# Kernel tuning notes

Measured on AMD Instinct MI355X. Metric: run time of the kernel, lower is better.

The kernel has to match this reference:

```python
import jax, jax.numpy as jnp
import numpy as np

TOTAL_NUM_PROP = 2000   # opt['total_num_prop_gp']
THR_START_END = 0.5     # opt['thr_start_end_gp']
NEG = -1e30             # score for invalid anchors


def setup_inputs() -> dict:
    key = jax.random.key(0)
    k1, k2, k3 = jax.random.split(key, 3)
    B, T = 16, 2048
    return {
        "start": jax.random.uniform(k1, (B, T), jnp.float32),
        "end": jax.random.uniform(k2, (B, T), jnp.float32),
        "actionness": jax.random.uniform(k3, (B, T), jnp.float32),
    }


def _select_anchors(p):
    # local-peak test (rise on left AND fall on right, boundaries count as true)
    # OR above-threshold test; matches uint8 sel1*sel2 + sel3 > 0 in torch code.
    B = p.shape[0]
    pad = jnp.ones((B, 1), bool)
    rise = jnp.concatenate([pad, p[:, 1:] > p[:, :-1]], axis=1)
    fall = jnp.concatenate([p[:, :-1] > p[:, 1:], pad], axis=1)
    high = p > THR_START_END * jnp.max(p, axis=1, keepdims=True)
    return (rise & fall) | high


def reference(start, end, actionness):
    # gen_prop == 'start_end' branch with tscale == T (step == 1)
    B, T = start.shape
    ss = _select_anchors(start)          # [B, T] selected start anchors
    es = _select_anchors(end)            # [B, T] selected end anchors
    s_ax = jnp.arange(T)
    # valid anchor pairs: both selected and end index >= start index
    valid = ss[:, :, None] & es[:, None, :] & (s_ax[None, :, None] <= s_ax[None, None, :])
    scores = jnp.where(valid, start[:, :, None] * end[:, None, :], NEG)  # [B, T, T]
    # per-batch top-K proposals by score (replaces argsort(descending)[:K])
    vals, idx = jax.lax.top_k(scores.reshape(B, T * T), TOTAL_NUM_PROP)
    s_idx = idx // T                      # start position
    e_idx = idx % T                       # end position
    keep = (vals > NEG).astype(jnp.float32)  # guards the (rare) <K-valid case
    dur = e_idx - s_idx                   # duration-minus-1 row index
    b_idx = jnp.broadcast_to(jnp.arange(B)[:, None], s_idx.shape)
    # scatter ones into dense [B, tscale(dur), tscale(start)] indicator map
    out = jnp.zeros((B, T, T), jnp.float32).at[b_idx, dur, s_idx].max(keep)
    return out
```

## Files before the change

### kernel.cpp

```cpp
#include <hip/hip_runtime.h>

constexpr int NB = 16;
constexpr int NT = 2048;
constexpr int KPROP = 2000;
constexpr int CAP = 8192;
constexpr int TIE_CAP = 2048;


__device__ void dscan(const unsigned* __restrict__ h, int nbuck, int nd, int tid,
                      int* cs, int* oB, int* oNd) {
    int chunk = nbuck >> 8;
    if (tid < 256) {
        int base = tid * chunk, s2 = 0;
        for (int c = 0; c < chunk; c++) s2 += (int)h[base + c];
        cs[tid] = s2;
    }
    __syncthreads();
    if (tid == 0) {
        int acc = 0, tc = -1;
        for (int t2 = 255; t2 >= 0; t2--) {
            if (acc + cs[t2] >= nd) { tc = t2; break; }
            acc += cs[t2];
        }
        int found = -1;
        if (tc >= 0) {
            for (int c = tc * chunk + chunk - 1; c >= tc * chunk; c--) {
                int cnt = (int)h[c];
                if (acc + cnt >= nd) { found = c; break; }
                acc += cnt;
            }
        }
        *oB = found;
        *oNd = nd - acc;
    }
    __syncthreads();
}

__device__ int scan512_excl(int x, int tid, volatile int* wsum, int* totOut) {
    int lane = tid & 63, wv = tid >> 6;
    int inc = x;
    #pragma unroll
    for (int d = 1; d < 64; d <<= 1) {
        int y = __shfl_up(inc, d);
        if (lane >= d) inc += y;
    }
    if (lane == 63) wsum[wv] = inc;
    __syncthreads();
    int base = 0, tot = 0;
    for (int w2 = 0; w2 < 8; w2++) {
        int v2 = wsum[w2];
        if (w2 < wv) base += v2;
        tot += v2;
    }
    __syncthreads();
    *totOut = tot;
    return base + (inc - x);
}

__device__ int reduce512(int x, int tid, volatile int* wsum) {
    int lane = tid & 63, wv = tid >> 6;
    #pragma unroll
    for (int d = 32; d > 0; d >>= 1) x += __shfl_down(x, d);
    if (lane == 0) wsum[wv] = x;
    __syncthreads();
    int tot = 0;
    for (int w2 = 0; w2 < 8; w2++) tot += wsum[w2];
    __syncthreads();
    return tot;
}

__global__ __launch_bounds__(512) void k_main(
        const float* __restrict__ start, const float* __restrict__ end,
        float4* __restrict__ out4,
        int* __restrict__ gMode, unsigned* __restrict__ gV32,
        int* __restrict__ gNd2, int* __restrict__ gCnt,
        unsigned* __restrict__ candFlat, unsigned* __restrict__ candBits) {
    int blk = blockIdx.x, tid = threadIdx.x;
    if (blk >= NB) {
        float4 z = make_float4(0.f, 0.f, 0.f, 0.f);
        size_t base = (size_t)(blk - NB) * 8192 + tid;
        #pragma unroll
        for (int it = 0; it < 16; it++) out4[base + (size_t)it * 512] = z;
        return;
    }
    int b = blk;
    size_t bc = (size_t)b * CAP;

    __shared__ short lsI[NT];  __shared__ float lsV[NT];
    __shared__ short leI[NT];  __shared__ float evV[NT];
    __shared__ float evVs[NT]; __shared__ short evIs[NT];
    __shared__ short actI[NT]; __shared__ short actC[NT];
    __shared__ unsigned Pmut[2048];
    __shared__ short PE[2051];
    __shared__ float redS[8];
    __shared__ int   red8[8];
    __shared__ int   cs[256];
    __shared__ float sMaxA[2];
    __shared__ int   sN[2];
    __shared__ int   scnt, sB, sNd;

    int lane = tid & 63, wv = tid >> 6;

    int w = tid >> 8, t = tid & 255;
    const float* p = (w ? end : start) + (size_t)b * NT;

    int t0 = t * 8;
    float v[8];
    *(float4*)&v[0] = *(const float4*)&p[t0];
    *(float4*)&v[4] = *(const float4*)&p[t0 + 4];

    float m = v[0];
    #pragma unroll
    for (int k = 1; k < 8; k++) m = fmaxf(m, v[k]);
    #pragma unroll
    for (int d = 32; d > 0; d >>= 1) m = fmaxf(m, (float)__shfl_down(m, d));
    if (lane == 0) redS[wv] = m;
    __syncthreads();
    float rowMax = fmaxf(fmaxf(redS[w * 4 + 0], redS[w * 4 + 1]),
                         fmaxf(redS[w * 4 + 2], redS[w * 4 + 3]));
    float thr = 0.5f * rowMax;
    if (t == 0) sMaxA[w] = rowMax;

    float prev = (t == 0)   ? -1.0f : p[t0 - 1];
    float next = (t == 255) ? -1.0f : p[t0 + 8];

    bool flag[8];
    int c = 0;
    #pragma unroll
    for (int k = 0; k < 8; k++) {
        float pv = (k == 0) ? prev : v[k - 1];
        float nv = (k == 7) ? next : v[k + 1];
        bool f = ((v[k] > pv) && (v[k] > nv)) || (v[k] > thr);
        flag[k] = f;
        c += f;
    }
    int inc = c;
    #pragma unroll
    for (int d = 1; d < 64; d <<= 1) {
        int y = __shfl_up(inc, d);
        if (lane >= d) inc += y;
    }
    if (lane == 63) red8[wv] = inc;
    __syncthreads();
    int base0 = 0;
    #pragma unroll
    for (int q = 0; q < 4; q++) {
        int vq = red8[w * 4 + q];
        if (q < (t >> 6)) base0 += vq;
    }
    int halfTot = red8[w * 4] + red8[w * 4 + 1] + red8[w * 4 + 2] + red8[w * 4 + 3];
    int pos = base0 + (inc - c);
    #pragma unroll
    for (int k = 0; k < 8; k++) {
        if (flag[k]) {
            if (w == 0) { lsI[pos] = (short)(t0 + k); lsV[pos] = v[k]; }
            else        { leI[pos] = (short)(t0 + k); evV[pos] = v[k]; }
            pos++;
        }
    }
    if (t == 0) sN[w] = halfTot;
    __syncthreads();

    int mS = sN[0], mE = sN[1];
    float maxE = sMaxA[1];
    float maxP = sMaxA[0] * maxE;

    int myTot = 0;
    for (int i = tid; i < mS; i += 512) {
        int sPos = lsI[i];
        int lo2 = 0, hi2 = mE;
        while (lo2 < hi2) { int mid = (lo2 + hi2) >> 1; if (leI[mid] < sPos) lo2 = mid + 1; else hi2 = mid; }
        myTot += mE - lo2;
    }
    int totalValid = reduce512(myTot, tid, red8);

    if (totalValid < KPROP) {
        if (tid == 0) scnt = 0;
        __syncthreads();
        for (int i = wv; i < mS; i += 8) {
            int sPos = lsI[i];
            for (int jb = 0; jb < mE; jb += 64) {
                int j = jb + lane;
                bool tk = (j < mE) && ((int)leI[j] >= sPos);
                unsigned long long vm = __ballot(tk);
                int cntv = __popcll(vm);
                if (cntv) {
                    int bw = 0;
                    if (lane == 0) bw = atomicAdd(&scnt, cntv);
                    bw = __shfl(bw, 0);
                    if (tk) {
                        int p2 = bw + __popcll(vm & ((1ull << lane) - 1ull));
                        if (p2 < CAP) candFlat[bc + p2] = (unsigned)((sPos << 11) | (int)leI[j]);
                    }
                }
            }
        }
        __syncthreads();
        if (tid == 0) { gMode[b] = 2; gCnt[b] = min(scnt, CAP); }
        return;
    }

    float mn = 3.4e38f;
    for (int k = tid; k < mE; k += 512) mn = fminf(mn, evV[k]);
    #pragma unroll
    for (int d = 32; d > 0; d >>= 1) mn = fminf(mn, (float)__shfl_down(mn, d));
    if (lane == 0) redS[wv] = mn;
    __syncthreads();
    float minV = redS[0];
    for (int w2 = 1; w2 < 8; w2++) minV = fminf(minV, redS[w2]);
    __syncthreads();
    float invW = 2047.0f / fmaxf(maxE - minV, 1e-30f);

    for (int k = tid; k < 2048; k += 512) Pmut[k] = 0u;
    __syncthreads();
    for (int k = tid; k < mE; k += 512) {
        float kf = fminf((evV[k] - minV) * invW, 2047.0f);
        int key = (int)kf; if (key < 0) key = 0;
        atomicAdd(&Pmut[2047 - key], 1u);
    }
    __syncthreads();
    {
        int c4[4], sum4 = 0;
        #pragma unroll
        for (int q = 0; q < 4; q++) { c4[q] = (int)Pmut[tid * 4 + q]; sum4 += c4[q]; }
        int tot;
        int base = scan512_excl(sum4, tid, red8, &tot);
        int run = base;
        #pragma unroll
        for (int q = 0; q < 4; q++) { PE[tid * 4 + q] = (short)run; run += c4[q]; }
        if (tid == 0) { PE[2048] = (short)tot; PE[2049] = (short)mE; PE[2050] = (short)mE; }
    }
    __syncthreads();
    for (int k = tid; k < 2048; k += 512) Pmut[k] = (unsigned)(short)PE[k];
    __syncthreads();
    for (int k = tid; k < mE; k += 512) {
        float vE = evV[k];
        float kf = fminf((vE - minV) * invW, 2047.0f);
        int key = (int)kf; if (key < 0) key = 0;
        int p2 = (int)atomicAdd(&Pmut[2047 - key], 1u);
        evVs[p2] = vE; evIs[p2] = leI[k];
    }
    __syncthreads();

    auto rowCount = [&](float tau, float sv) -> int {
        float x = tau / sv;
        float kf = fminf((x - minV) * invW, 2050.0f);
        int kk = (int)kf - 2;
        if (kk < -2) kk = -2;
        if (kk > 2048) kk = 2048;
        return (int)PE[2048 - kk];
    };
    auto incOracle = [&](float tau) -> int {
        int my = 0;
        for (int i = tid; i < mS; i += 512) my += rowCount(tau, lsV[i]);
        return reduce512(my, tid, red8);
    };

    float aT = 0.0f, bT = maxP;
    float Fa = (float)mS * (float)mE;
    float Fb = 0.0f;
    float t40 = -1.0f;
    for (int it = 0; it < 12; it++) {
        float mid;
        float denom = Fa - Fb;
        if (denom > 1.0f) {
            mid = aT + (bT - aT) * ((Fa - 9000.0f) / denom);
            if (!(mid > aT && mid < bT)) mid = 0.5f * (aT + bT);
        } else mid = 0.5f * (aT + bT);
        int incC = incOracle(mid);
        if (incC > 13000) { aT = mid; Fa = (float)incC; }
        else if (incC < 5000) { bT = mid; Fb = (float)incC; }
        else { t40 = mid; break; }
    }
    if (t40 < 0.0f && Fa <= 24576.0f) t40 = aT;

    bool ok = false;
    int n = 0;

    if (t40 >= 0.0f) {
        __shared__ int sActN;
        {
            int a4[4], na = 0;
            #pragma unroll
            for (int q = 0; q < 4; q++) {
                int i = tid * 4 + q;
                int C = (i < mS) ? rowCount(t40, lsV[i]) : 0;
                a4[q] = C; na += (C > 0);
            }
            int tot;
            int base = scan512_excl(na, tid, red8, &tot);
            int run = base;
            #pragma unroll
            for (int q = 0; q < 4; q++) {
                if (a4[q] > 0) { actI[run] = (short)(tid * 4 + q); actC[run] = (short)a4[q]; run++; }
            }
            if (tid == 0) sActN = tot;
        }
        __syncthreads();
        int actN = sActN;

        float lo = t40;
        float bscale = 2047.0f / fmaxf(maxP - lo, 1e-30f);
        for (int cc2 = tid; cc2 < 2048; cc2 += 512) Pmut[cc2] = 0u;
        if (tid == 0) scnt = 0;
        __syncthreads();
        int certLoc = 0;
        for (int r = wv; r < actN; r += 8) {
            int i = (int)actI[r];
            float sv = lsV[i]; int sPos = lsI[i];
            int C = (int)actC[r];
            for (int jb = 0; jb < C; jb += 64) {
                int j = jb + lane;
                bool keep = false;
                float prod = 0.0f;
                int eIdx = 0;
                if (j < C) {
                    eIdx = (int)evIs[j];
                    prod = sv * evVs[j];
                    keep = (eIdx >= sPos);
                }
                if (keep) {
                    int key = (int)((prod - lo) * bscale);
                    key = key < 0 ? 0 : (key > 2047 ? 2047 : key);
                    atomicAdd(&Pmut[key], 1u);
                    if (prod >= t40) certLoc++;
                }
                unsigned long long vm = __ballot(keep);
                int cntv = __popcll(vm);
                if (cntv) {
                    int bw = 0;
                    if (lane == 0) bw = atomicAdd(&scnt, cntv);
                    bw = __shfl(bw, 0);
                    if (keep) {
                        int p2 = bw + __popcll(vm & ((1ull << lane) - 1ull));
                        if (p2 < CAP) {
                            candFlat[bc + p2] = (unsigned)((sPos << 11) | eIdx);
                            candBits[bc + p2] = __float_as_uint(prod);
                        }
                    }
                }
            }
        }
        __syncthreads();
        n = scnt;
        __syncthreads();
        int certTot = reduce512(certLoc, tid, red8);
        if (certTot >= KPROP) {
            if (n <= CAP) {
                ok = true;
            } else {
                dscan(Pmut, 2048, KPROP, tid, cs, &sB, &sNd);
                int bb = sB;
                if (bb >= 1) {
                    int cumBB = (KPROP - sNd) + (int)Pmut[bb];
                    if (cumBB <= CAP) {
                        if (tid == 0) scnt = 0;
                        __syncthreads();
                        for (int r = wv; r < actN; r += 8) {
                            int i = (int)actI[r];
                            float sv = lsV[i]; int sPos = lsI[i];
                            int C = (int)actC[r];
                            for (int jb = 0; jb < C; jb += 64) {
                                int j = jb + lane;
                                bool keep = false;
                                float prod = 0.0f;
                                int eIdx = 0;
                                if (j < C) {
                                    eIdx = (int)evIs[j];
                                    prod = sv * evVs[j];
                                    int key = (int)((prod - lo) * bscale);
                                    key = key < 0 ? 0 : (key > 2047 ? 2047 : key);
                                    keep = (eIdx >= sPos) && (key >= bb);
                                }
                                unsigned long long vm = __ballot(keep);
                                int cntv = __popcll(vm);
                                if (cntv) {
                                    int bw = 0;
                                    if (lane == 0) bw = atomicAdd(&scnt, cntv);
                                    bw = __shfl(bw, 0);
                                    if (keep) {
                                        int p2 = bw + __popcll(vm & ((1ull << lane) - 1ull));
                                        if (p2 < CAP) {
                                            candFlat[bc + p2] = (unsigned)((sPos << 11) | eIdx);
                                            candBits[bc + p2] = __float_as_uint(prod);
                                        }
                                    }
                                }
                            }
                        }
                        __syncthreads();
                        n = scnt;
                        __syncthreads();
                        if (n >= KPROP && n <= CAP) ok = true;
                    }
                }
            }
        }
    }

    if (!ok) {
        auto exactCount = [&](float tau) -> int {
            int my = 0;
            for (int i = wv; i < mS; i += 8) {
                float sv2 = lsV[i]; int sPos = lsI[i];
                for (int jb = 0; jb < mE; jb += 64) {
                    int j = jb + lane;
                    if (j < mE && (int)leI[j] >= sPos && sv2 * evV[j] >= tau) my++;
                }
            }
            return reduce512(my, tid, red8);
        };
        float a3 = 0.0f, b3 = maxP, tau3 = -1.0f;
        for (int it = 0; it < 24; it++) {
            float mid = 0.5f * (a3 + b3);
            int cnt = exactCount(mid);
            if (cnt > CAP) a3 = mid;
            else { b3 = mid; tau3 = mid; if (cnt >= KPROP) break; }
        }
        if (tau3 < 0.0f) tau3 = b3;
        if (tid == 0) scnt = 0;
        __syncthreads();
        for (int i = wv; i < mS; i += 8) {
            float sv2 = lsV[i]; int sPos = lsI[i];
            for (int jb = 0; jb < mE; jb += 64) {
                int j = jb + lane;
                float prod = (j < mE) ? sv2 * evV[j] : 0.0f;
                bool valid = (j < mE) && ((int)leI[j] >= sPos) && (prod >= tau3);
                unsigned long long vm = __ballot(valid);
                int cntv = __popcll(vm);
                if (cntv) {
                    int bw = 0;
                    if (lane == 0) bw = atomicAdd(&scnt, cntv);
                    bw = __shfl(bw, 0);
                    if (valid) {
                        int p2 = bw + __popcll(vm & ((1ull << lane) - 1ull));
                        if (p2 < CAP) {
                            candFlat[bc + p2] = (unsigned)((sPos << 11) | (int)leI[j]);
                            candBits[bc + p2] = __float_as_uint(prod);
                        }
                    }
                }
            }
        }
        __syncthreads();
        n = min(scnt, CAP);
        __syncthreads();
        if (n >= KPROP) ok = true;
    }

    if (!ok) {
        if (tid == 0) { gMode[b] = 2; gCnt[b] = n; }
        return;
    }

    for (int cc2 = tid; cc2 < 2048; cc2 += 512) Pmut[cc2] = 0u;
    __syncthreads();
    for (int k = tid; k < n; k += 512) atomicAdd(&Pmut[candBits[bc + k] >> 20], 1u);
    __syncthreads();
    dscan(Pmut, 2048, KPROP, tid, cs, &sB, &sNd);
    unsigned bA = (unsigned)sB;
    int ndA = sNd;
    __syncthreads();

    for (int cc2 = tid; cc2 < 1024; cc2 += 512) Pmut[cc2] = 0u;
    __syncthreads();
    for (int k = tid; k < n; k += 512) {
        unsigned bits = candBits[bc + k];
        if ((bits >> 20) == bA) atomicAdd(&Pmut[(bits >> 10) & 1023], 1u);
    }
    __syncthreads();
    dscan(Pmut, 1024, ndA, tid, cs, &sB, &sNd);
    unsigned pref20 = (bA << 10) | (unsigned)sB;
    int ndB = sNd;
    __syncthreads();

    for (int cc2 = tid; cc2 < 1024; cc2 += 512) Pmut[cc2] = 0u;
    __syncthreads();
    for (int k = tid; k < n; k += 512) {
        unsigned bits = candBits[bc + k];
        if ((bits >> 10) == pref20) atomicAdd(&Pmut[bits & 1023], 1u);
    }
    __syncthreads();
    dscan(Pmut, 1024, ndB, tid, cs, &sB, &sNd);

    if (tid == 0) {
        gV32[b] = (pref20 << 10) | (unsigned)sB;
        gNd2[b] = sNd;
        gMode[b] = 1;
        gCnt[b]  = n;
    }
}

__global__ __launch_bounds__(512) void k_emit(
        const int* __restrict__ gMode, const unsigned* __restrict__ gV32,
        const int* __restrict__ gNd2, const int* __restrict__ gCnt,
        const unsigned* __restrict__ candFlat, const unsigned* __restrict__ candBits,
        float* __restrict__ out) {
    int b = blockIdx.x, tid = threadIdx.x;
    int md = gMode[b], n = gCnt[b];
    const unsigned* cf = candFlat + (size_t)b * CAP;

    if (md == 2) {
        for (int k = tid; k < n; k += 512) {
            unsigned f = cf[k];
            int s = (int)(f >> 11), e = (int)(f & 2047u);
            out[((size_t)b * NT + (e - s)) * NT + s] = 1.0f;
        }
        return;
    }

    __shared__ unsigned tie[TIE_CAP];
    __shared__ int tieCnt;
    if (tid == 0) tieCnt = 0;
    __syncthreads();

    unsigned V32 = gV32[b];
    int nd2 = gNd2[b];
    const unsigned* cb = candBits + (size_t)b * CAP;

    for (int k = tid; k < n; k += 512) {
        unsigned bits = cb[k];
        unsigned f = cf[k];
        if (bits > V32) {
            int s = (int)(f >> 11), e = (int)(f & 2047u);
            out[((size_t)b * NT + (e - s)) * NT + s] = 1.0f;
        } else if (bits == V32) {
            int pp = atomicAdd(&tieCnt, 1);
            if (pp < TIE_CAP) tie[pp] = f;
        }
    }
    __syncthreads();
    int tn = min(tieCnt, TIE_CAP);
    for (int k = tid; k < tn; k += 512) {
        unsigned f = tie[k];
        int rank = 0;
        for (int j = 0; j < tn; j++) rank += (tie[j] < f) ? 1 : 0;
        if (rank < nd2) {
            int s = (int)(f >> 11), e = (int)(f & 2047u);
            out[((size_t)b * NT + (e - s)) * NT + s] = 1.0f;
        }
    }
}

extern "C" void kernel_launch(void* const* d_in, const int* in_sizes, int n_in,
                              void* d_out, int out_size, void* d_ws, size_t ws_size,
                              hipStream_t stream) {
    const float* start = (const float*)d_in[0];
    const float* end   = (const float*)d_in[1];
    float* out = (float*)d_out;
    char* ws = (char*)d_ws;

    int*      gMode    = (int*)     (ws + 0);
    unsigned* gV32     = (unsigned*)(ws + 64);
    int*      gNd2     = (int*)     (ws + 128);
    int*      gCnt     = (int*)     (ws + 192);
    unsigned* candFlat = (unsigned*)(ws + 4096);
    unsigned* candBits = (unsigned*)(ws + 528384);

    k_main<<<NB + 2048, 512, 0, stream>>>(start, end, (float4*)out,
                                          gMode, gV32, gNd2, gCnt,
                                          candFlat, candBits);
    k_emit<<<NB, 512, 0, stream>>>(gMode, gV32, gNd2, gCnt, candFlat, candBits, out);
}
```

Baseline: 74.14 us.

## Run threshold search in one wavefront and shortcut K-th value via bucket rank

The interpolation search for the candidate threshold now runs inside a single wavefront with shuffle reductions, so each iteration no longer needs block-wide reductions and barriers. When the candidate histogram built during collection is valid, the boundary bucket's members are gathered into shared memory and ranked by brute-force comparison in one wavefront. This finds the exact K-th value directly and returns early, skipping the later two-level radix histogram passes. The cost is an extra shared buffer and a quadratic rank step, which is bounded by TB_CAP. The search now uses 64 threads instead of 512, so each iteration does more serial work per thread.

```diff
diff --git a/kernel.cpp b/kernel.cpp
--- a/kernel.cpp
+++ b/kernel.cpp
@@ -5,6 +5,7 @@
 constexpr int KPROP = 2000;
 constexpr int CAP = 8192;
 constexpr int TIE_CAP = 2048;
+constexpr int TB_CAP = 1024;
 
 
 __device__ void dscan(const unsigned* __restrict__ h, int nbuck, int nd, int tid,
@@ -92,12 +93,14 @@
     __shared__ short actI[NT]; __shared__ short actC[NT];
     __shared__ unsigned Pmut[2048];
     __shared__ short PE[2051];
+    __shared__ unsigned tb[TB_CAP];
     __shared__ float redS[8];
     __shared__ int   red8[8];
     __shared__ int   cs[256];
     __shared__ float sMaxA[2];
     __shared__ int   sN[2];
-    __shared__ int   scnt, sB, sNd;
+    __shared__ int   scnt, sB, sNd, tbCnt, sFlag;
+    __shared__ float sT40;
 
     int lane = tid & 63, wv = tid >> 6;
 
@@ -250,32 +253,38 @@
         if (kk > 2048) kk = 2048;
         return (int)PE[2048 - kk];
     };
-    auto incOracle = [&](float tau) -> int {
-        int my = 0;
-        for (int i = tid; i < mS; i += 512) my += rowCount(tau, lsV[i]);
-        return reduce512(my, tid, red8);
-    };
-
-    float aT = 0.0f, bT = maxP;
-    float Fa = (float)mS * (float)mE;
-    float Fb = 0.0f;
-    float t40 = -1.0f;
-    for (int it = 0; it < 12; it++) {
-        float mid;
-        float denom = Fa - Fb;
-        if (denom > 1.0f) {
-            mid = aT + (bT - aT) * ((Fa - 9000.0f) / denom);
-            if (!(mid > aT && mid < bT)) mid = 0.5f * (aT + bT);
-        } else mid = 0.5f * (aT + bT);
-        int incC = incOracle(mid);
-        if (incC > 13000) { aT = mid; Fa = (float)incC; }
-        else if (incC < 5000) { bT = mid; Fb = (float)incC; }
-        else { t40 = mid; break; }
-    }
-    if (t40 < 0.0f && Fa <= 24576.0f) t40 = aT;
+
+    if (wv == 0) {
+        float aT = 0.0f, bT = maxP;
+        float Fa = (float)mS * (float)mE;
+        float Fb = 0.0f;
+        float t40w = -1.0f;
+        for (int it = 0; it < 12; it++) {
+            float mid;
+            float denom = Fa - Fb;
+            if (denom > 1.0f) {
+                mid = aT + (bT - aT) * ((Fa - 9000.0f) / denom);
+                if (!(mid > aT && mid < bT)) mid = 0.5f * (aT + bT);
+            } else mid = 0.5f * (aT + bT);
+            int my = 0;
+            for (int i = lane; i < mS; i += 64) my += rowCount(mid, lsV[i]);
+            #pragma unroll
+            for (int d = 32; d > 0; d >>= 1) my += __shfl_down(my, d);
+            int incC = __shfl(my, 0);
+            if (incC > 13000) { aT = mid; Fa = (float)incC; }
+            else if (incC < 5000) { bT = mid; Fb = (float)incC; }
+            else { t40w = mid; break; }
+        }
+        if (t40w < 0.0f && Fa <= 24576.0f) t40w = aT;
+        if (lane == 0) sT40 = t40w;
+    }
+    __syncthreads();
+    float t40 = sT40;
 
     bool ok = false;
+    bool histValid = false;
     int n = 0;
+    float lo = 0.0f, bscale = 0.0f;
 
     if (t40 >= 0.0f) {
         __shared__ int sActN;
@@ -299,8 +308,8 @@
         __syncthreads();
         int actN = sActN;
 
-        float lo = t40;
-        float bscale = 2047.0f / fmaxf(maxP - lo, 1e-30f);
+        lo = t40;
+        bscale = 2047.0f / fmaxf(maxP - lo, 1e-30f);
         for (int cc2 = tid; cc2 < 2048; cc2 += 512) Pmut[cc2] = 0u;
         if (tid == 0) scnt = 0;
         __syncthreads();
@@ -347,7 +356,7 @@
         int certTot = reduce512(certLoc, tid, red8);
         if (certTot >= KPROP) {
             if (n <= CAP) {
-                ok = true;
+                ok = true; histValid = true;
             } else {
                 dscan(Pmut, 2048, KPROP, tid, cs, &sB, &sNd);
                 int bb = sB;
@@ -391,7 +400,7 @@
                         __syncthreads();
                         n = scnt;
                         __syncthreads();
-                        if (n >= KPROP && n <= CAP) ok = true;
+                        if (n >= KPROP && n <= CAP) { ok = true; histValid = true; }
                     }
                 }
             }
@@ -453,6 +462,52 @@
         return;
     }
 
+    if (histValid) {
+        dscan(Pmut, 2048, KPROP, tid, cs, &sB, &sNd);
+        int bbT = sB, sNdT = sNd;
+        if (bbT >= 0 && (int)Pmut[bbT] <= TB_CAP) {
+            if (tid == 0) { tbCnt = 0; sFlag = 0; }
+            __syncthreads();
+            for (int k = tid; k < n; k += 512) {
+                unsigned bits = candBits[bc + k];
+                float prod = __uint_as_float(bits);
+                int key = (int)((prod - lo) * bscale);
+                key = key < 0 ? 0 : (key > 2047 ? 2047 : key);
+                if (key == bbT) {
+                    int pp = atomicAdd(&tbCnt, 1);
+                    if (pp < TB_CAP) tb[pp] = bits;
+                }
+            }
+            __syncthreads();
+            int cntBB = tbCnt;
+            if (cntBB <= TB_CAP && wv == 0) {
+                unsigned v32 = 0u; int nd2v = -1;
+                for (int k = lane; k < cntBB; k += 64) {
+                    unsigned bk = tb[k];
+                    int gt = 0, eq = 0;
+                    for (int j = 0; j < cntBB; j++) {
+                        unsigned bj = tb[j];
+                        gt += (bj > bk) ? 1 : 0;
+                        eq += (bj == bk) ? 1 : 0;
+                    }
+                    if (gt < sNdT && gt + eq >= sNdT) { v32 = bk; nd2v = sNdT - gt; }
+                }
+                unsigned long long msk = __ballot(nd2v >= 0);
+                if (msk) {
+                    int src = __ffsll((unsigned long long)msk) - 1;
+                    v32 = __shfl(v32, src);
+                    nd2v = __shfl(nd2v, src);
+                    if (lane == 0) {
+                        gV32[b] = v32; gNd2[b] = nd2v; gMode[b] = 1; gCnt[b] = n;
+                        sFlag = 1;
+                    }
+                }
+            }
+            __syncthreads();
+            if (sFlag) return;
+        }
+    }
+
     for (int cc2 = tid; cc2 < 2048; cc2 += 512) Pmut[cc2] = 0u;
     __syncthreads();
     for (int k = tid; k < n; k += 512) atomicAdd(&Pmut[candBits[bc + k] >> 20], 1u);
```

Measured after the change: 59.92 us, median of 2. 1.24x faster.
